# Performance work log

Measured on AMD Instinct MI355X. Metric: run time of the kernel, lower is better.

## Reference

```python
import jax, jax.numpy as jnp
import numpy as np
import math

N = 100000      # nodes
E = 1600000     # edges
D = 128         # in_channels
C = 256         # number of dominant-set cliques
HID = 64        # mlp_hidden
RATIO = 0.8
K = int(math.ceil(RATIO * N))  # 80000 topk nodes per view


def setup_inputs() -> dict:
    key = jax.random.key(0)
    ks = jax.random.split(key, 18)
    s = 0.05
    return {
        "x": jax.random.normal(ks[0], (N, D), jnp.float32),
        "edge_index": jax.random.randint(ks[1], (2, E), 0, N, dtype=jnp.int32),
        "batch": jnp.zeros((N,), jnp.int32),
        "cluster_id": jax.random.randint(ks[2], (N,), 0, C, dtype=jnp.int32),
        # MLP scorer: Linear(D,HID) -> ReLU -> Linear(HID,1)
        "mlp_w1": jax.random.normal(ks[3], (D, HID), jnp.float32) * s,
        "mlp_b1": jnp.zeros((HID,), jnp.float32),
        "mlp_w2": jax.random.normal(ks[4], (HID, 1), jnp.float32) * s,
        "mlp_b2": jnp.zeros((1,), jnp.float32),
        # GATConv(D, 1, heads=1)
        "gat_w": jax.random.normal(ks[5], (D, 1), jnp.float32) * s,
        "gat_a_src": jax.random.normal(ks[6], (1,), jnp.float32) * s,
        "gat_a_dst": jax.random.normal(ks[7], (1,), jnp.float32) * s,
        "gat_b": jnp.zeros((1,), jnp.float32),
        # InterChannelGCN attention Linear(2D,1) split into fine/coarse halves
        "att_w_fine": jax.random.normal(ks[8], (D,), jnp.float32) * s,
        "att_w_coarse": jax.random.normal(ks[9], (D,), jnp.float32) * s,
        "att_b": jnp.zeros((1,), jnp.float32),
        # InterChannelGCN transform Linear(D,D)
        "trans_w": jax.random.normal(ks[10], (D, D), jnp.float32) * s,
        "trans_b": jnp.zeros((D,), jnp.float32),
    }


def _inter_channel_gcn(h_fine, H_coarse, R, wa, wb, ab, tw, tb):
    # attention(Linear(2D,1)) on concat(h_fine_i, H_coarse_j) == h_fine@wa + H_coarse@wb + b
    scores = h_fine @ wa[:, None] + (H_coarse @ wb)[None, :] + ab[0]   # [K, C]
    attn = jax.nn.softmax(scores * R, axis=-1)                          # mask-by-multiply, as original
    out = attn @ H_coarse + h_fine                                      # add_self=True
    return jax.nn.relu(out @ tw + tb)                                   # normalize=False


def reference(x, edge_index, batch, cluster_id,
              mlp_w1, mlp_b1, mlp_w2, mlp_b2,
              gat_w, gat_a_src, gat_a_dst, gat_b,
              att_w_fine, att_w_coarse, att_b, trans_w, trans_b):
    src, dst = edge_index[0], edge_index[1]

    # --- DominantClustering('avg'): cluster means as coarse features ---
    counts = jax.ops.segment_sum(jnp.ones((N,), jnp.float32), cluster_id, num_segments=C)
    Hcoarse = jax.ops.segment_sum(x, cluster_id, num_segments=C) / jnp.maximum(counts, 1.0)[:, None]

    # --- feature view: MLP score + topk ---
    feature_score = (jax.nn.relu(x @ mlp_w1 + mlp_b1) @ mlp_w2 + mlp_b2)[:, 0]   # [N]
    _, feat_idx = jax.lax.top_k(feature_score, K)
    feature_view3 = x[feat_idx]
    R_feat = jax.nn.one_hot(cluster_id[feat_idx], C, dtype=x.dtype)              # relationship matrix
    fuse1 = _inter_channel_gcn(feature_view3, Hcoarse, R_feat,
                               att_w_fine, att_w_coarse, att_b, trans_w, trans_b)

    # --- local view: GATConv(D,1,heads=1) score + topk ---
    h = x @ gat_w                                                                 # [N,1]
    e = jax.nn.leaky_relu(gat_a_src[0] * h[src, 0] + gat_a_dst[0] * h[dst, 0], 0.2)  # [E]
    m = jax.ops.segment_max(e, dst, num_segments=N)
    ex = jnp.exp(e - m[dst])
    den = jax.ops.segment_sum(ex, dst, num_segments=N)
    alpha = ex / jnp.maximum(den[dst], 1e-16)
    localview_score = jax.ops.segment_sum(alpha * h[src, 0], dst, num_segments=N) + gat_b[0]
    _, local_idx = jax.lax.top_k(localview_score, K)
    local_view1 = x[local_idx]
    R_local = jax.nn.one_hot(cluster_id[local_idx], C, dtype=x.dtype)
    fuse2 = _inter_channel_gcn(local_view1, Hcoarse, R_local,
                               att_w_fine, att_w_coarse, att_b, trans_w, trans_b)

    # --- union, edge filtering + remapping (padded fixed shapes) ---
    in_feat = jnp.zeros((N,), bool).at[feat_idx].set(True)
    in_local = jnp.zeros((N,), bool).at[local_idx].set(True)
    union = in_feat | in_local
    mapping = jnp.where(union, jnp.cumsum(union.astype(jnp.int32)) - 1, -1)
    m0, m1 = mapping[src], mapping[dst]
    valid = (m0 >= 0) & (m1 >= 0)
    edge_index_topk = jnp.where(valid[None, :], jnp.stack([m0, m1]), -1)          # [2,E], -1 = dropped

    # --- fused features (faithful to original's fuse1/fuse2 index swap) ---
    A = jnp.zeros((N, D), x.dtype).at[feat_idx].set(fuse2)    # fuse2 indexed by feature topk position
    B = jnp.zeros((N, D), x.dtype).at[local_idx].set(fuse1)   # fuse1 indexed by local topk position
    both = in_feat & in_local
    Fp = jnp.where(both[:, None], (A + B) * 0.5, A + B)
    Fp = jnp.where(union[:, None], Fp, 0.0)                   # [N,D], zero outside union

    new_batch = jnp.where(union, batch, -1)
    return Fp, edge_index_topk, new_batch
```

## Files before the change

### kernel.cpp

```cpp
#include <hip/hip_runtime.h>
#include <hip/hip_bf16.h>
#include <stdint.h>

#define N 100000
#define E_ 1600000
#define D 128
#define C_ 256
#define HID 64
#define KSEL 80000
#define NB 4096
#define CHUNK 1024
#define NCHUNK ((N + CHUNK - 1) / CHUNK)
#define CSEG 32
#define NBK 782
#define BCAP 2560
#define RMAX 2048
#define NSC64 ((N + 63) / 64)
#define EB ((E_ + 255) / 256)
#define ZB ((N * 32 + 255) / 256)

typedef __attribute__((ext_vector_type(8))) short bf16x8;
typedef __attribute__((ext_vector_type(4))) float f32x4;

__device__ __forceinline__ unsigned enc_f(float f) {
  unsigned b = __float_as_uint(f);
  return (b & 0x80000000u) ? ~b : (b | 0x80000000u);
}
__device__ __forceinline__ float dec_f(unsigned u) {
  unsigned b = (u & 0x80000000u) ? (u ^ 0x80000000u) : ~u;
  return __uint_as_float(b);
}

__device__ __forceinline__ unsigned short f2bf(float f) {
  unsigned u = __float_as_uint(f);
  unsigned r = u + 0x7FFFu + ((u >> 16) & 1u);
  return (unsigned short)(r >> 16);
}

__global__ __launch_bounds__(256) void k_hist_cluster(const int* __restrict__ cid, int* __restrict__ ccount) {
  int n = blockIdx.x * 256 + threadIdx.x;
  if (n < N) atomicAdd(&ccount[cid[n]], 1);
}

__global__ __launch_bounds__(1024) void k_scan_small(const int* __restrict__ in0, int* __restrict__ out0, int n) {
  __shared__ int sums[1024];
  const int* in = in0 + (size_t)blockIdx.x * n;
  int* out = out0 + (size_t)blockIdx.x * n;
  int t = threadIdx.x;
  int per = (n + 1023) / 1024;
  int base = t * per;
  int loc = 0;
  for (int k = 0; k < per; ++k) { int i = base + k; if (i < n) loc += in[i]; }
  sums[t] = loc; __syncthreads();
  for (int off = 1; off < 1024; off <<= 1) {
    int v = (t >= off) ? sums[t - off] : 0;
    __syncthreads();
    sums[t] += v;
    __syncthreads();
  }
  int run = (t == 0) ? 0 : sums[t - 1];
  for (int k = 0; k < per; ++k) { int i = base + k; if (i < n) { out[i] = run; run += in[i]; } }
}

__global__ __launch_bounds__(256) void k_scatter_cluster(const int* __restrict__ cid, const int* __restrict__ cstart,
                                                         int* __restrict__ ccur, int* __restrict__ cslot) {
  int n = blockIdx.x * 256 + threadIdx.x;
  if (n < N) {
    int c = cid[n];
    int p = cstart[c] + atomicAdd(&ccur[c], 1);
    cslot[p] = n;
  }
}

__global__ __launch_bounds__(128) void k_cluster_partial(const float* __restrict__ x, const int* __restrict__ cstart,
                                                         const int* __restrict__ ccount, const int* __restrict__ cslot,
                                                         float* __restrict__ Hc) {
  int c = blockIdx.x >> 5;
  int s = blockIdx.x & (CSEG - 1);
  int d = threadIdx.x;
  int st = cstart[c], cnt = ccount[c];
  int seg = (cnt + CSEG - 1) / CSEG;
  int lo = s * seg;
  int hi = min(cnt, lo + seg);
  if (lo >= hi) return;
  float acc = 0.f;
  int k = lo;
  for (; k + 2 <= hi; k += 2) {
    int n0 = cslot[st + k], n1 = cslot[st + k + 1];
    float v0 = x[(size_t)n0 * D + d];
    float v1 = x[(size_t)n1 * D + d];
    acc += v0 + v1;
  }
  if (k < hi) acc += x[(size_t)cslot[st + k] * D + d];
  atomicAdd(&Hc[(size_t)c * D + d], acc);
}

__global__ __launch_bounds__(128) void k_mean_gdot(const int* __restrict__ ccount, const float* __restrict__ wb,
                                                   float* __restrict__ Hc, float* __restrict__ gdot) {
  __shared__ float red[128];
  int c = blockIdx.x, d = threadIdx.x;
  float hv = Hc[(size_t)c * D + d] / (float)max(ccount[c], 1);
  Hc[(size_t)c * D + d] = hv;
  red[d] = hv * wb[d];
  __syncthreads();
  if (d < 64) {
    float v = red[d] + red[d + 64];
    for (int off = 32; off; off >>= 1) v += __shfl_down(v, off);
    if (d == 0) gdot[c] = v;
  }
}

__global__ __launch_bounds__(128) void k_S_SW_HW(const float* __restrict__ Hc, const float* __restrict__ tw,
                                                 float* __restrict__ SW, float* __restrict__ HW,
                                                 unsigned short* __restrict__ twT) {
  __shared__ float Sl[128];
  int b = blockIdx.x, t = threadIdx.x;
  if (b == 0) {
    float s = 0.f;
    for (int c = 0; c < C_; ++c) s += Hc[(size_t)c * D + t];
    Sl[t] = s;
    __syncthreads();
    float acc = 0.f;
    for (int d = 0; d < D; ++d) acc = fmaf(Sl[d], tw[(size_t)d * D + t], acc);
    SW[t] = acc;
  } else if (b <= C_) {
    const float* src = Hc + (size_t)(b - 1) * D;
    float acc = 0.f;
    for (int d = 0; d < D; ++d) acc = fmaf(src[d], tw[(size_t)d * D + t], acc);
    HW[(size_t)(b - 1) * D + t] = acc;
  } else {
    int k = b - C_ - 1;
    twT[(size_t)t * D + k] = f2bf(tw[(size_t)k * D + t]);
  }
}

__global__ __launch_bounds__(256, 4) void k_score64(const float* __restrict__ x, const float* __restrict__ w1,
                                                    const float* __restrict__ b1, const float* __restrict__ w2,
                                                    const float* __restrict__ b2, const float* __restrict__ gw,
                                                    const float* __restrict__ wa, float* __restrict__ scoreF,
                                                    float* __restrict__ hg, float* __restrict__ aDot,
                                                    uint2* __restrict__ pmmF) {
  __shared__ float xld[64 * D];
  int tid = threadIdx.x;
  int base = blockIdx.x * 64;
#pragma unroll
  for (int k = 0; k < 8; ++k) {
    int i = k * 256 + tid;
    int r = i >> 5, cc = i & 31;
    int n = base + r;
    float4 v = make_float4(0.f, 0.f, 0.f, 0.f);
    if (n < N) v = ((const float4*)(x + (size_t)n * D))[cc];
    ((float4*)xld)[r * 32 + (cc ^ (r & 7))] = v;
  }
  __syncthreads();

  int rg = tid >> 4;
  int cg = tid & 15;
  int r0 = rg * 4;
  int c4 = cg * 4;
  float acc[4][4] = {};
  float4 wc0 = *(const float4*)(w1 + (size_t)0 * HID + c4);
  float4 wc1 = *(const float4*)(w1 + (size_t)1 * HID + c4);
  float4 wc2 = *(const float4*)(w1 + (size_t)2 * HID + c4);
  float4 wc3 = *(const float4*)(w1 + (size_t)3 * HID + c4);
  for (int d4 = 0; d4 < D; d4 += 4) {
    float4 wn0, wn1, wn2, wn3;
    if (d4 + 4 < D) {
      wn0 = *(const float4*)(w1 + (size_t)(d4 + 4) * HID + c4);
      wn1 = *(const float4*)(w1 + (size_t)(d4 + 5) * HID + c4);
      wn2 = *(const float4*)(w1 + (size_t)(d4 + 6) * HID + c4);
      wn3 = *(const float4*)(w1 + (size_t)(d4 + 7) * HID + c4);
    } else {
      wn0 = wn1 = wn2 = wn3 = make_float4(0.f, 0.f, 0.f, 0.f);
    }
    int j = d4 >> 2;
#pragma unroll
    for (int rr = 0; rr < 4; ++rr) {
      int row = r0 + rr;
      float4 xv = ((const float4*)xld)[row * 32 + (j ^ (row & 7))];
      acc[rr][0] = fmaf(xv.x, wc0.x, acc[rr][0]);
      acc[rr][1] = fmaf(xv.x, wc0.y, acc[rr][1]);
      acc[rr][2] = fmaf(xv.x, wc0.z, acc[rr][2]);
      acc[rr][3] = fmaf(xv.x, wc0.w, acc[rr][3]);
      acc[rr][0] = fmaf(xv.y, wc1.x, acc[rr][0]);
      acc[rr][1] = fmaf(xv.y, wc1.y, acc[rr][1]);
      acc[rr][2] = fmaf(xv.y, wc1.z, acc[rr][2]);
      acc[rr][3] = fmaf(xv.y, wc1.w, acc[rr][3]);
      acc[rr][0] = fmaf(xv.z, wc2.x, acc[rr][0]);
      acc[rr][1] = fmaf(xv.z, wc2.y, acc[rr][1]);
      acc[rr][2] = fmaf(xv.z, wc2.z, acc[rr][2]);
      acc[rr][3] = fmaf(xv.z, wc2.w, acc[rr][3]);
      acc[rr][0] = fmaf(xv.w, wc3.x, acc[rr][0]);
      acc[rr][1] = fmaf(xv.w, wc3.y, acc[rr][1]);
      acc[rr][2] = fmaf(xv.w, wc3.z, acc[rr][2]);
      acc[rr][3] = fmaf(xv.w, wc3.w, acc[rr][3]);
    }
    wc0 = wn0; wc1 = wn1; wc2 = wn2; wc3 = wn3;
  }

  float4 b1v = *(const float4*)(b1 + c4);
  float4 w2v = *(const float4*)(w2 + c4);
  float bb = b2[0];
  unsigned vmx = 0u, vmn = 0xFFFFFFFFu;
#pragma unroll
  for (int rr = 0; rr < 4; ++rr) {
    float p = fmaxf(acc[rr][0] + b1v.x, 0.f) * w2v.x
            + fmaxf(acc[rr][1] + b1v.y, 0.f) * w2v.y
            + fmaxf(acc[rr][2] + b1v.z, 0.f) * w2v.z
            + fmaxf(acc[rr][3] + b1v.w, 0.f) * w2v.w;
#pragma unroll
    for (int off = 8; off; off >>= 1) p += __shfl_xor(p, off);
    if (cg == 0) {
      int n = base + r0 + rr;
      if (n < N) {
        float sf = p + bb;
        scoreF[n] = sf;
        unsigned e = enc_f(sf);
        vmx = max(vmx, e);
        vmn = min(vmn, e);
      }
    }
  }
#pragma unroll
  for (int off = 32; off; off >>= 1) {
    vmx = max(vmx, (unsigned)__shfl_xor((int)vmx, off));
    vmn = min(vmn, (unsigned)__shfl_xor((int)vmn, off));
  }

  float4 gwa = *(const float4*)(gw + c4);
  float4 gwb = *(const float4*)(gw + 64 + c4);
  float4 waa = *(const float4*)(wa + c4);
  float4 wab = *(const float4*)(wa + 64 + c4);
#pragma unroll
  for (int rr = 0; rr < 4; ++rr) {
    int row = r0 + rr;
    float4 xa = ((const float4*)xld)[row * 32 + (cg ^ (row & 7))];
    float4 xb = ((const float4*)xld)[row * 32 + ((cg + 16) ^ (row & 7))];
    float hp = xa.x * gwa.x + xa.y * gwa.y + xa.z * gwa.z + xa.w * gwa.w
             + xb.x * gwb.x + xb.y * gwb.y + xb.z * gwb.z + xb.w * gwb.w;
    float ap = xa.x * waa.x + xa.y * waa.y + xa.z * waa.z + xa.w * waa.w
             + xb.x * wab.x + xb.y * wab.y + xb.z * wab.z + xb.w * wab.w;
#pragma unroll
    for (int off = 8; off; off >>= 1) {
      hp += __shfl_xor(hp, off);
      ap += __shfl_xor(ap, off);
    }
    if (cg == 0) {
      int n = base + row;
      if (n < N) { hg[n] = hp; aDot[n] = ap; }
    }
  }

  __syncthreads();
  if ((tid & 63) == 0) {
    ((unsigned*)xld)[(tid >> 6) * 2] = vmx;
    ((unsigned*)xld)[(tid >> 6) * 2 + 1] = vmn;
  }
  __syncthreads();
  if (tid == 0) {
    const unsigned* xu = (const unsigned*)xld;
    unsigned a = max(max(xu[0], xu[2]), max(xu[4], xu[6]));
    unsigned b = min(min(xu[1], xu[3]), min(xu[5], xu[7]));
    pmmF[blockIdx.x] = make_uint2(a, b);
  }
}

__global__ __launch_bounds__(1024) void k_escatter(const int* __restrict__ ei, int* __restrict__ gcnt,
                                                   unsigned* __restrict__ payload) {
  __shared__ int lcnt[NBK];
  __shared__ int lbase[NBK];
  int tid = threadIdx.x;
  for (int i = tid; i < NBK; i += 1024) lcnt[i] = 0;
  int e0 = blockIdx.x * 8192;
  int es[8], ed[8];
#pragma unroll
  for (int k = 0; k < 8; ++k) {
    int e = e0 + k * 1024 + tid;
    bool v = (e < E_);
    es[k] = v ? ei[e] : -1;
    ed[k] = v ? ei[E_ + e] : -1;
  }
  __syncthreads();
#pragma unroll
  for (int k = 0; k < 8; ++k)
    if (ed[k] >= 0) atomicAdd(&lcnt[ed[k] >> 7], 1);
  __syncthreads();
  for (int i = tid; i < NBK; i += 1024) {
    int c = lcnt[i];
    lbase[i] = c ? atomicAdd(&gcnt[i], c) : 0;
    lcnt[i] = 0;
  }
  __syncthreads();
#pragma unroll
  for (int k = 0; k < 8; ++k) {
    if (ed[k] < 0) continue;
    int s = es[k], d = ed[k];
    int b = d >> 7, dl = d & 127;
    int pos = lbase[b] + atomicAdd(&lcnt[b], 1);
    if (pos < BCAP) payload[(size_t)b * BCAP + pos] = (unsigned)s | ((unsigned)dl << 24);
  }
}

__global__ __launch_bounds__(256) void k_esoftmax(const unsigned* __restrict__ payload, const int* __restrict__ gcnt,
                                                  const float* __restrict__ hg, const float* __restrict__ asrc,
                                                  const float* __restrict__ adst, const float* __restrict__ gb,
                                                  float* __restrict__ scoreL, uint2* __restrict__ pmmL) {
  __shared__ float dS[128];
  __shared__ float nS[128];
  __shared__ float hgl[128];
  __shared__ unsigned pw[8];
  int b = blockIdx.x;
  int tid = threadIdx.x;
  if (tid < 128) {
    dS[tid] = 0.f; nS[tid] = 0.f;
    int g = b * 128 + tid;
    hgl[tid] = (g < N) ? hg[g] : 0.f;
  }
  __syncthreads();
  float as = asrc[0], ad = adst[0];
  int cnt = min(gcnt[b], BCAP);
  const unsigned* bp = payload + (size_t)b * BCAP;
  for (int i = tid; i < cnt; i += 256) {
    unsigned r = bp[i];
    int s = (int)(r & 0xFFFFFFu), dl = (int)(r >> 24);
    float h = hg[s];
    float z = as * h + ad * hgl[dl];
    float ev = (z > 0.f) ? z : 0.2f * z;
    float ex = expf(ev);
    atomicAdd(&dS[dl], ex);
    atomicAdd(&nS[dl], ex * h);
  }
  __syncthreads();
  unsigned vmx = 0u, vmn = 0xFFFFFFFFu;
  if (tid < 128) {
    int dst = b * 128 + tid;
    if (dst < N) {
      float sl = nS[tid] / fmaxf(dS[tid], 1e-16f) + gb[0];
      scoreL[dst] = sl;
      unsigned e = enc_f(sl);
      vmx = e; vmn = e;
    }
  }
#pragma unroll
  for (int off = 32; off; off >>= 1) {
    vmx = max(vmx, (unsigned)__shfl_xor((int)vmx, off));
    vmn = min(vmn, (unsigned)__shfl_xor((int)vmn, off));
  }
  if ((tid & 63) == 0) { pw[(tid >> 6) * 2] = vmx; pw[(tid >> 6) * 2 + 1] = vmn; }
  __syncthreads();
  if (tid == 0) {
    unsigned a = max(max(pw[0], pw[2]), max(pw[4], pw[6]));
    unsigned c = min(min(pw[1], pw[3]), min(pw[5], pw[7]));
    pmmL[b] = make_uint2(a, c);
  }
}

__global__ __launch_bounds__(1024) void k_mm_reduce(const uint2* __restrict__ pmmF, const uint2* __restrict__ pmmL,
                                                    unsigned* __restrict__ mm) {
  __shared__ unsigned s[4][16];
  int t = threadIdx.x;
  unsigned mxF = 0u, mnF = 0xFFFFFFFFu, mxL = 0u, mnL = 0xFFFFFFFFu;
  for (int i = t; i < NSC64; i += 1024) {
    uint2 v = pmmF[i];
    mxF = max(mxF, v.x); mnF = min(mnF, v.y);
  }
  for (int i = t; i < NBK; i += 1024) {
    uint2 v = pmmL[i];
    mxL = max(mxL, v.x); mnL = min(mnL, v.y);
  }
#pragma unroll
  for (int off = 32; off; off >>= 1) {
    mxF = max(mxF, (unsigned)__shfl_xor((int)mxF, off));
    mnF = min(mnF, (unsigned)__shfl_xor((int)mnF, off));
    mxL = max(mxL, (unsigned)__shfl_xor((int)mxL, off));
    mnL = min(mnL, (unsigned)__shfl_xor((int)mnL, off));
  }
  int w = t >> 6;
  if ((t & 63) == 0) { s[0][w] = mxF; s[1][w] = mnF; s[2][w] = mxL; s[3][w] = mnL; }
  __syncthreads();
  if (t == 0) {
    unsigned a = 0u, b = 0xFFFFFFFFu, c = 0u, d = 0xFFFFFFFFu;
    for (int i = 0; i < 16; ++i) {
      a = max(a, s[0][i]); b = min(b, s[1][i]);
      c = max(c, s[2][i]); d = min(d, s[3][i]);
    }
    mm[0] = a; mm[2] = b; mm[1] = c; mm[3] = d;
  }
}

__global__ __launch_bounds__(256) void k_bucket_hist2(const float* __restrict__ sc2, const unsigned* __restrict__ mm,
                                                      int* __restrict__ bucket2, int* __restrict__ hist2) {
  int v = blockIdx.y;
  int n = blockIdx.x * 256 + threadIdx.x;
  if (n >= N) return;
  const float* sc = sc2 + (size_t)v * N;
  float smax = dec_f(mm[v]), smin = dec_f(mm[2 + v]);
  float range = smax - smin;
  float scale = (range > 0.f) ? ((float)NB / range) : 0.f;
  float t = (smax - sc[n]) * scale;
  int b = (int)t;
  b = b < 0 ? 0 : (b > NB - 1 ? NB - 1 : b);
  bucket2[(size_t)v * N + n] = b;
  atomicAdd(&hist2[v * NB + b], 1);
}

__global__ __launch_bounds__(256) void k_bucket_scatter2(const int* __restrict__ bucket2, const int* __restrict__ start2,
                                                         int* __restrict__ cur2, int* __restrict__ slot2) {
  int v = blockIdx.y;
  int n = blockIdx.x * 256 + threadIdx.x;
  if (n >= N) return;
  int b = bucket2[(size_t)v * N + n];
  slot2[(size_t)v * N + start2[v * NB + b] + atomicAdd(&cur2[v * NB + b], 1)] = n;
}

__global__ __launch_bounds__(64) void k_bucket_rank3(const float* __restrict__ sc2, const int* __restrict__ start2,
                                                     const int* __restrict__ hist2, const int* __restrict__ slot2,
                                                     int* __restrict__ rank2, int* __restrict__ sorted2) {
  __shared__ unsigned long long keys[RMAX];
  int v = blockIdx.y;
  int b = blockIdx.x;
  int st = start2[v * NB + b], cnt = hist2[v * NB + b];
  if (cnt == 0) return;
  const float* sc = sc2 + (size_t)v * N;
  const int* slot = slot2 + (size_t)v * N;
  int* rank = rank2 + (size_t)v * N;
  int* sorted = sorted2 + (size_t)v * N;
  int tid = threadIdx.x;
  if (cnt <= RMAX) {
    for (int i = tid; i < cnt; i += 64) {
      int m = slot[st + i];
      keys[i] = (((unsigned long long)(~enc_f(sc[m]))) << 32) | (unsigned)m;
    }
    __syncthreads();
    for (int i = tid; i < cnt; i += 64) {
      unsigned long long mykey = keys[i];
      int r = 0;
      for (int j = 0; j < cnt; ++j) r += (keys[j] < mykey) ? 1 : 0;
      int m = (int)(mykey & 0xFFFFFFFFu);
      rank[m] = st + r;
      sorted[st + r] = m;
    }
  } else {
    for (int i = tid; i < cnt; i += 64) {
      int m = slot[st + i];
      unsigned long long mykey = (((unsigned long long)(~enc_f(sc[m]))) << 32) | (unsigned)m;
      int r = 0;
      for (int j = 0; j < cnt; ++j) {
        int mj = slot[st + j];
        unsigned long long k = (((unsigned long long)(~enc_f(sc[mj]))) << 32) | (unsigned)mj;
        r += (k < mykey) ? 1 : 0;
      }
      rank[m] = st + r;
      sorted[st + r] = m;
    }
  }
}

__global__ __launch_bounds__(1024) void k_union_chunksum(const int* __restrict__ rankF, const int* __restrict__ rankL,
                                                         int* __restrict__ csum) {
  __shared__ int red[1024];
  int t = threadIdx.x; int i = blockIdx.x * 1024 + t;
  int u = (i < N) ? (((rankF[i] < KSEL) || (rankL[i] < KSEL)) ? 1 : 0) : 0;
  red[t] = u; __syncthreads();
  for (int off = 512; off; off >>= 1) { if (t < off) red[t] += red[t + off]; __syncthreads(); }
  if (t == 0) csum[blockIdx.x] = red[0];
}

__global__ __launch_bounds__(1024) void k_union_map(const int* __restrict__ rankF, const int* __restrict__ rankL,
                                                    const int* __restrict__ cstart, const int* __restrict__ batch,
                                                    int* __restrict__ mapping, float* __restrict__ outBatch) {
  __shared__ int sums[1024];
  int t = threadIdx.x; int i = blockIdx.x * 1024 + t;
  int u = (i < N) ? (((rankF[i] < KSEL) || (rankL[i] < KSEL)) ? 1 : 0) : 0;
  sums[t] = u; __syncthreads();
  for (int off = 1; off < 1024; off <<= 1) {
    int v = (t >= off) ? sums[t - off] : 0;
    __syncthreads();
    sums[t] += v;
    __syncthreads();
  }
  if (i < N) {
    mapping[i] = u ? (cstart[blockIdx.x] + sums[t] - 1) : -1;
    outBatch[i] = u ? (float)batch[i] : -1.0f;
  }
}

__global__ __launch_bounds__(256) void k_edge_zero(const int* __restrict__ ei, const int* __restrict__ mapping,
                                                   float* __restrict__ outE, float* __restrict__ Fp) {
  int b = blockIdx.x;
  if (b < EB) {
    int e = b * 256 + threadIdx.x;
    if (e >= E_) return;
    int m0 = mapping[ei[e]], m1 = mapping[ei[E_ + e]];
    bool valid = (m0 >= 0) && (m1 >= 0);
    outE[e] = valid ? (float)m0 : -1.f;
    outE[E_ + e] = valid ? (float)m1 : -1.f;
  } else {
    int i = (b - EB) * 256 + threadIdx.x;
    int n = i >> 5;
    if (n < N && mapping[n] < 0) ((float4*)Fp)[i] = make_float4(0.f, 0.f, 0.f, 0.f);
  }
}

__global__ __launch_bounds__(256, 4) void k_fuse64(const float* __restrict__ x, const unsigned short* __restrict__ twT,
                                                   const float* __restrict__ tb, const float* __restrict__ SW,
                                                   const float* __restrict__ HW, const float* __restrict__ gdot,
                                                   const float* __restrict__ aDot, const int* __restrict__ cid,
                                                   const int* __restrict__ srcL, const int* __restrict__ tgtL,
                                                   const float* __restrict__ attb, const int* __restrict__ rankF,
                                                   float* __restrict__ Fp, int accum) {
  __shared__ __align__(16) unsigned xw[64 * 64];
  __shared__ float pq[64 * 2];
  __shared__ int mt[64 * 2];
  __shared__ int ft[64];
  int tid = threadIdx.x;
  int base = blockIdx.x * 64;
  if (tid < 64) {
    int ws = srcL[base + tid];
    int cc = cid[ws];
    int tg = tgtL[base + tid];
    mt[tid * 2] = cc;
    mt[tid * 2 + 1] = tg;
    ft[tid] = (rankF[tg] < KSEL) ? 1 : 0;
    float s = aDot[ws] + gdot[cc] + attb[0];
    float mx = fmaxf(s, 0.f);
    float esm = expf(s - mx), eom = expf(-mx);
    float dn = esm + 255.f * eom;
    pq[tid * 2] = esm / dn;
    pq[tid * 2 + 1] = eom / dn;
  }
#pragma unroll
  for (int k = 0; k < 8; ++k) {
    int i = k * 256 + tid;
    int r = i >> 5, c4 = i & 31;
    int ws = srcL[base + r];
    float4 v = ((const float4*)(x + (size_t)ws * D))[c4];
    uint2 pk;
    pk.x = (unsigned)f2bf(v.x) | ((unsigned)f2bf(v.y) << 16);
    pk.y = (unsigned)f2bf(v.z) | ((unsigned)f2bf(v.w) << 16);
    int u2 = r * 32 + (c4 ^ ((r & 7) << 1));
    ((uint2*)xw)[u2] = pk;
  }
  __syncthreads();

  int w = tid >> 6;
  int l = tid & 63;
  int nl = l & 15;
  int khalf = l >> 4;
  int row = w * 16 + nl;

  f32x4 acc[8] = {};
  const char* xbase = (const char*)xw + row * 256;
  unsigned rsw = (unsigned)((row & 7) << 4);
  bf16x8 bfr[4];
#pragma unroll
  for (int ks = 0; ks < 4; ++ks)
    bfr[ks] = *(const bf16x8*)(xbase + (((unsigned)(ks * 64 + khalf * 16)) ^ rsw));
#pragma unroll
  for (int ks = 0; ks < 4; ++ks) {
#pragma unroll
    for (int ot = 0; ot < 8; ++ot) {
      bf16x8 afrag = *(const bf16x8*)(twT + (size_t)(ot * 16 + nl) * D + ks * 32 + khalf * 8);
      acc[ot] = __builtin_amdgcn_mfma_f32_16x16x32_bf16(afrag, bfr[ks], acc[ot], 0, 0, 0);
    }
  }

  float p = pq[row * 2], q = pq[row * 2 + 1];
  int cc = mt[row * 2];
  int tgt = mt[row * 2 + 1];
  int doAcc = accum && ft[row];
#pragma unroll
  for (int ot = 0; ot < 8; ++ot) {
    int ch = ot * 16 + khalf * 4;
    float4 tbv = *(const float4*)(tb + ch);
    float4 swv = *(const float4*)(SW + ch);
    float4 hw = *(const float4*)(HW + (size_t)cc * D + ch);
    float4 o;
    o.x = fmaxf(acc[ot][0] + tbv.x + q * swv.x + (p - q) * hw.x, 0.f);
    o.y = fmaxf(acc[ot][1] + tbv.y + q * swv.y + (p - q) * hw.y, 0.f);
    o.z = fmaxf(acc[ot][2] + tbv.z + q * swv.z + (p - q) * hw.z, 0.f);
    o.w = fmaxf(acc[ot][3] + tbv.w + q * swv.w + (p - q) * hw.w, 0.f);
    float4* dst = (float4*)(Fp + (size_t)tgt * D + ch);
    if (doAcc) {
      float4 old = *dst;
      o.x = (o.x + old.x) * 0.5f;
      o.y = (o.y + old.y) * 0.5f;
      o.z = (o.z + old.z) * 0.5f;
      o.w = (o.w + old.w) * 0.5f;
    }
    *dst = o;
  }
}

extern "C" void kernel_launch(void* const* d_in, const int* in_sizes, int n_in,
                              void* d_out, int out_size, void* d_ws, size_t ws_size,
                              hipStream_t stream) {
  const float* x   = (const float*)d_in[0];
  const int* ei    = (const int*)d_in[1];
  const int* batch = (const int*)d_in[2];
  const int* cid   = (const int*)d_in[3];
  const float* w1  = (const float*)d_in[4];
  const float* b1  = (const float*)d_in[5];
  const float* w2  = (const float*)d_in[6];
  const float* b2  = (const float*)d_in[7];
  const float* gw  = (const float*)d_in[8];
  const float* gas = (const float*)d_in[9];
  const float* gad = (const float*)d_in[10];
  const float* gb  = (const float*)d_in[11];
  const float* wa  = (const float*)d_in[12];
  const float* wb  = (const float*)d_in[13];
  const float* ab  = (const float*)d_in[14];
  const float* tw  = (const float*)d_in[15];
  const float* tb  = (const float*)d_in[16];
  (void)in_sizes; (void)n_in; (void)ws_size; (void)out_size;

  char* p = (char*)d_ws;
  auto alloc = [&](size_t bytes) -> char* {
    char* r = p;
    p += (bytes + 255) & ~(size_t)255;
    return r;
  };
  int* ccount    = (int*)alloc(C_ * 4);
  int* ccur      = (int*)alloc(C_ * 4);
  unsigned* mm   = (unsigned*)alloc(16);
  int* hist2     = (int*)alloc(2 * NB * 4);
  int* cur2      = (int*)alloc(2 * NB * 4);
  float* Hc      = (float*)alloc((size_t)C_ * D * 4);
  int* gcnt      = (int*)alloc(NBK * 4);
  size_t zeroBytes = (size_t)(p - (char*)d_ws);
  int* cstart   = (int*)alloc(C_ * 4);
  int* cslot    = (int*)alloc((size_t)N * 4);
  float* gdot   = (float*)alloc(C_ * 4);
  float* SW     = (float*)alloc(D * 4);
  float* HW     = (float*)alloc((size_t)C_ * D * 4);
  unsigned short* twT = (unsigned short*)alloc((size_t)D * D * 2);
  float* score2 = (float*)alloc((size_t)2 * N * 4);
  float* hg     = (float*)alloc((size_t)N * 4);
  float* aDot   = (float*)alloc((size_t)N * 4);
  unsigned* payload = (unsigned*)alloc((size_t)NBK * BCAP * 4);
  uint2* pmmF   = (uint2*)alloc((size_t)NSC64 * 8);
  uint2* pmmL   = (uint2*)alloc((size_t)NBK * 8);
  int* bucket2  = (int*)alloc((size_t)2 * N * 4);
  int* start2   = (int*)alloc(2 * NB * 4);
  int* slot2    = (int*)alloc((size_t)2 * N * 4);
  int* sorted2  = (int*)alloc((size_t)2 * N * 4);
  int* rank2    = (int*)alloc((size_t)2 * N * 4);
  int* csums    = (int*)alloc(NCHUNK * 4);
  int* cstarts  = (int*)alloc(NCHUNK * 4);
  int* mapping  = (int*)alloc((size_t)N * 4);

  float* scoreF = score2;
  float* scoreL = score2 + N;
  int* sortedF  = sorted2;
  int* sortedL  = sorted2 + N;
  int* rankF    = rank2;
  int* rankL    = rank2 + N;

  float* outF = (float*)d_out;
  float* outE = outF + (size_t)N * D;
  float* outB = outE + (size_t)2 * E_;

  hipMemsetAsync(d_ws, 0, zeroBytes, stream);

  k_hist_cluster<<<(N + 255) / 256, 256, 0, stream>>>(cid, ccount);
  k_scan_small<<<1, 1024, 0, stream>>>(ccount, cstart, C_);
  k_scatter_cluster<<<(N + 255) / 256, 256, 0, stream>>>(cid, cstart, ccur, cslot);
  k_cluster_partial<<<C_ * CSEG, 128, 0, stream>>>(x, cstart, ccount, cslot, Hc);
  k_mean_gdot<<<C_, 128, 0, stream>>>(ccount, wb, Hc, gdot);
  k_S_SW_HW<<<C_ + 1 + D, 128, 0, stream>>>(Hc, tw, SW, HW, twT);

  k_score64<<<NSC64, 256, 0, stream>>>(x, w1, b1, w2, b2, gw, wa, scoreF, hg, aDot, pmmF);
  k_escatter<<<(E_ + 8191) / 8192, 1024, 0, stream>>>(ei, gcnt, payload);
  k_esoftmax<<<NBK, 256, 0, stream>>>(payload, gcnt, hg, gas, gad, gb, scoreL, pmmL);
  k_mm_reduce<<<1, 1024, 0, stream>>>(pmmF, pmmL, mm);

  dim3 g2((N + 255) / 256, 2);
  k_bucket_hist2<<<g2, 256, 0, stream>>>(score2, mm, bucket2, hist2);
  k_scan_small<<<2, 1024, 0, stream>>>(hist2, start2, NB);
  k_bucket_scatter2<<<g2, 256, 0, stream>>>(bucket2, start2, cur2, slot2);
  dim3 gr(NB, 2);
  k_bucket_rank3<<<gr, 64, 0, stream>>>(score2, start2, hist2, slot2, rank2, sorted2);

  k_union_chunksum<<<NCHUNK, 1024, 0, stream>>>(rankF, rankL, csums);
  k_scan_small<<<1, 1024, 0, stream>>>(csums, cstarts, NCHUNK);
  k_union_map<<<NCHUNK, 1024, 0, stream>>>(rankF, rankL, cstarts, batch, mapping, outB);
  k_edge_zero<<<EB + ZB, 256, 0, stream>>>(ei, mapping, outE, outF);

  k_fuse64<<<KSEL / 64, 256, 0, stream>>>(x, twT, tb, SW, HW, gdot, aDot, cid, sortedL, sortedF, ab, rankF, outF, 0);
  k_fuse64<<<KSEL / 64, 256, 0, stream>>>(x, twT, tb, SW, HW, gdot, aDot, cid, sortedF, sortedL, ab, rankF, outF, 1);
}
```

Measured before the change: 520.7 us.

## Fuse two fuse passes into one union-indexed kernel computing both views per node

Builds a compacted list of union nodes during the mapping step. A single kernel then walks that list and, for each target node, computes both the fine and coarse-view transforms and averages them in registers. This replaces two launches, one of which read back the first pass's output for averaging. In exchange, every union node runs both MFMA passes, including nodes that belong to only one view, and shared memory use doubles.

```diff
diff --git a/kernel.cpp b/kernel.cpp
--- a/kernel.cpp
+++ b/kernel.cpp
@@ -468,7 +468,8 @@
 
 __global__ __launch_bounds__(1024) void k_union_map(const int* __restrict__ rankF, const int* __restrict__ rankL,
                                                     const int* __restrict__ cstart, const int* __restrict__ batch,
-                                                    int* __restrict__ mapping, float* __restrict__ outBatch) {
+                                                    int* __restrict__ mapping, float* __restrict__ outBatch,
+                                                    int* __restrict__ ulist) {
   __shared__ int sums[1024];
   int t = threadIdx.x; int i = blockIdx.x * 1024 + t;
   int u = (i < N) ? (((rankF[i] < KSEL) || (rankL[i] < KSEL)) ? 1 : 0) : 0;
@@ -480,7 +481,9 @@
     __syncthreads();
   }
   if (i < N) {
-    mapping[i] = u ? (cstart[blockIdx.x] + sums[t] - 1) : -1;
+    int m_ = u ? (cstart[blockIdx.x] + sums[t] - 1) : -1;
+    mapping[i] = m_;
+    if (u) ulist[m_] = i;
     outBatch[i] = u ? (float)batch[i] : -1.0f;
   }
 }
@@ -502,44 +505,74 @@
   }
 }
 
-__global__ __launch_bounds__(256, 4) void k_fuse64(const float* __restrict__ x, const unsigned short* __restrict__ twT,
-                                                   const float* __restrict__ tb, const float* __restrict__ SW,
-                                                   const float* __restrict__ HW, const float* __restrict__ gdot,
-                                                   const float* __restrict__ aDot, const int* __restrict__ cid,
-                                                   const int* __restrict__ srcL, const int* __restrict__ tgtL,
-                                                   const float* __restrict__ attb, const int* __restrict__ rankF,
-                                                   float* __restrict__ Fp, int accum) {
-  __shared__ __align__(16) unsigned xw[64 * 64];
-  __shared__ float pq[64 * 2];
-  __shared__ int mt[64 * 2];
-  __shared__ int ft[64];
+__global__ __launch_bounds__(256) void k_fuseU(const float* __restrict__ x, const unsigned short* __restrict__ twT,
+                                               const float* __restrict__ tb, const float* __restrict__ SW,
+                                               const float* __restrict__ HW, const float* __restrict__ gdot,
+                                               const float* __restrict__ aDot, const int* __restrict__ cid,
+                                               const int* __restrict__ sortedF, const int* __restrict__ sortedL,
+                                               const int* __restrict__ rankF, const int* __restrict__ rankL,
+                                               const int* __restrict__ ulist, const int* __restrict__ cstarts,
+                                               const int* __restrict__ csums, const float* __restrict__ attb,
+                                               float* __restrict__ Fp) {
+  __shared__ __align__(16) unsigned xwA[64 * 64];
+  __shared__ __align__(16) unsigned xwB[64 * 64];
+  __shared__ float pqA[64 * 2], pqB[64 * 2];
+  __shared__ int mtA[64], mtB[64];
+  __shared__ int tgl[64];
+  __shared__ int fl[64];
+  __shared__ int srcAB[64 * 2];
   int tid = threadIdx.x;
   int base = blockIdx.x * 64;
+  int UC = cstarts[NCHUNK - 1] + csums[NCHUNK - 1];
+  if (base >= UC) return;
   if (tid < 64) {
-    int ws = srcL[base + tid];
-    int cc = cid[ws];
-    int tg = tgtL[base + tid];
-    mt[tid * 2] = cc;
-    mt[tid * 2 + 1] = tg;
-    ft[tid] = (rankF[tg] < KSEL) ? 1 : 0;
-    float s = aDot[ws] + gdot[cc] + attb[0];
-    float mx = fmaxf(s, 0.f);
-    float esm = expf(s - mx), eom = expf(-mx);
-    float dn = esm + 255.f * eom;
-    pq[tid * 2] = esm / dn;
-    pq[tid * 2 + 1] = eom / dn;
-  }
+    int pos = base + tid;
+    int t = (pos < UC) ? ulist[pos] : -1;
+    int ra = (t >= 0) ? rankF[t] : KSEL;
+    int rb = (t >= 0) ? rankL[t] : KSEL;
+    int vA = (ra < KSEL) ? 1 : 0;
+    int vB = (rb < KSEL) ? 1 : 0;
+    int sA = vA ? sortedL[ra] : 0;
+    int sB = vB ? sortedF[rb] : 0;
+    srcAB[tid * 2] = sA;
+    srcAB[tid * 2 + 1] = sB;
+    tgl[tid] = t;
+    fl[tid] = vA | (vB << 1);
+    int cA = cid[sA], cB = cid[sB];
+    mtA[tid] = cA;
+    mtB[tid] = cB;
+    float ab0 = attb[0];
+    float sAv = aDot[sA] + gdot[cA] + ab0;
+    float mxA = fmaxf(sAv, 0.f);
+    float eA = expf(sAv - mxA), oA = expf(-mxA);
+    float dA = eA + 255.f * oA;
+    pqA[tid * 2] = eA / dA;
+    pqA[tid * 2 + 1] = oA / dA;
+    float sBv = aDot[sB] + gdot[cB] + ab0;
+    float mxB = fmaxf(sBv, 0.f);
+    float eB = expf(sBv - mxB), oB = expf(-mxB);
+    float dB = eB + 255.f * oB;
+    pqB[tid * 2] = eB / dB;
+    pqB[tid * 2 + 1] = oB / dB;
+  }
+  __syncthreads();
 #pragma unroll
   for (int k = 0; k < 8; ++k) {
     int i = k * 256 + tid;
     int r = i >> 5, c4 = i & 31;
-    int ws = srcL[base + r];
-    float4 v = ((const float4*)(x + (size_t)ws * D))[c4];
+    int u2 = r * 32 + (c4 ^ ((r & 7) << 1));
+    int wsA = srcAB[r * 2];
+    float4 v = ((const float4*)(x + (size_t)wsA * D))[c4];
     uint2 pk;
     pk.x = (unsigned)f2bf(v.x) | ((unsigned)f2bf(v.y) << 16);
     pk.y = (unsigned)f2bf(v.z) | ((unsigned)f2bf(v.w) << 16);
-    int u2 = r * 32 + (c4 ^ ((r & 7) << 1));
-    ((uint2*)xw)[u2] = pk;
+    ((uint2*)xwA)[u2] = pk;
+    int wsB = srcAB[r * 2 + 1];
+    float4 u = ((const float4*)(x + (size_t)wsB * D))[c4];
+    uint2 pk2;
+    pk2.x = (unsigned)f2bf(u.x) | ((unsigned)f2bf(u.y) << 16);
+    pk2.y = (unsigned)f2bf(u.z) | ((unsigned)f2bf(u.w) << 16);
+    ((uint2*)xwB)[u2] = pk2;
   }
   __syncthreads();
 
@@ -549,46 +582,60 @@
   int khalf = l >> 4;
   int row = w * 16 + nl;
 
-  f32x4 acc[8] = {};
-  const char* xbase = (const char*)xw + row * 256;
+  f32x4 accA[8] = {};
+  f32x4 accB[8] = {};
+  const char* xbA = (const char*)xwA + row * 256;
+  const char* xbB = (const char*)xwB + row * 256;
   unsigned rsw = (unsigned)((row & 7) << 4);
-  bf16x8 bfr[4];
-#pragma unroll
-  for (int ks = 0; ks < 4; ++ks)
-    bfr[ks] = *(const bf16x8*)(xbase + (((unsigned)(ks * 64 + khalf * 16)) ^ rsw));
+  bf16x8 bfrA[4], bfrB[4];
+#pragma unroll
+  for (int ks = 0; ks < 4; ++ks) {
+    unsigned off = ((unsigned)(ks * 64 + khalf * 16)) ^ rsw;
+    bfrA[ks] = *(const bf16x8*)(xbA + off);
+    bfrB[ks] = *(const bf16x8*)(xbB + off);
+  }
 #pragma unroll
   for (int ks = 0; ks < 4; ++ks) {
 #pragma unroll
     for (int ot = 0; ot < 8; ++ot) {
       bf16x8 afrag = *(const bf16x8*)(twT + (size_t)(ot * 16 + nl) * D + ks * 32 + khalf * 8);
-      acc[ot] = __builtin_amdgcn_mfma_f32_16x16x32_bf16(afrag, bfr[ks], acc[ot], 0, 0, 0);
-    }
-  }
-
-  float p = pq[row * 2], q = pq[row * 2 + 1];
-  int cc = mt[row * 2];
-  int tgt = mt[row * 2 + 1];
-  int doAcc = accum && ft[row];
+      accA[ot] = __builtin_amdgcn_mfma_f32_16x16x32_bf16(afrag, bfrA[ks], accA[ot], 0, 0, 0);
+      accB[ot] = __builtin_amdgcn_mfma_f32_16x16x32_bf16(afrag, bfrB[ks], accB[ot], 0, 0, 0);
+    }
+  }
+
+  int t = tgl[row];
+  int f = fl[row];
+  float pA = pqA[row * 2], qA = pqA[row * 2 + 1];
+  float pB = pqB[row * 2], qB = pqB[row * 2 + 1];
+  int cA = mtA[row], cB = mtB[row];
 #pragma unroll
   for (int ot = 0; ot < 8; ++ot) {
     int ch = ot * 16 + khalf * 4;
     float4 tbv = *(const float4*)(tb + ch);
     float4 swv = *(const float4*)(SW + ch);
-    float4 hw = *(const float4*)(HW + (size_t)cc * D + ch);
-    float4 o;
-    o.x = fmaxf(acc[ot][0] + tbv.x + q * swv.x + (p - q) * hw.x, 0.f);
-    o.y = fmaxf(acc[ot][1] + tbv.y + q * swv.y + (p - q) * hw.y, 0.f);
-    o.z = fmaxf(acc[ot][2] + tbv.z + q * swv.z + (p - q) * hw.z, 0.f);
-    o.w = fmaxf(acc[ot][3] + tbv.w + q * swv.w + (p - q) * hw.w, 0.f);
-    float4* dst = (float4*)(Fp + (size_t)tgt * D + ch);
-    if (doAcc) {
-      float4 old = *dst;
-      o.x = (o.x + old.x) * 0.5f;
-      o.y = (o.y + old.y) * 0.5f;
-      o.z = (o.z + old.z) * 0.5f;
-      o.w = (o.w + old.w) * 0.5f;
-    }
-    *dst = o;
+    float4 hwA = *(const float4*)(HW + (size_t)cA * D + ch);
+    float4 hwB = *(const float4*)(HW + (size_t)cB * D + ch);
+    float4 oA, oB, o;
+    oA.x = fmaxf(accA[ot][0] + tbv.x + qA * swv.x + (pA - qA) * hwA.x, 0.f);
+    oA.y = fmaxf(accA[ot][1] + tbv.y + qA * swv.y + (pA - qA) * hwA.y, 0.f);
+    oA.z = fmaxf(accA[ot][2] + tbv.z + qA * swv.z + (pA - qA) * hwA.z, 0.f);
+    oA.w = fmaxf(accA[ot][3] + tbv.w + qA * swv.w + (pA - qA) * hwA.w, 0.f);
+    oB.x = fmaxf(accB[ot][0] + tbv.x + qB * swv.x + (pB - qB) * hwB.x, 0.f);
+    oB.y = fmaxf(accB[ot][1] + tbv.y + qB * swv.y + (pB - qB) * hwB.y, 0.f);
+    oB.z = fmaxf(accB[ot][2] + tbv.z + qB * swv.z + (pB - qB) * hwB.z, 0.f);
+    oB.w = fmaxf(accB[ot][3] + tbv.w + qB * swv.w + (pB - qB) * hwB.w, 0.f);
+    if (f == 3) {
+      o.x = (oA.x + oB.x) * 0.5f;
+      o.y = (oA.y + oB.y) * 0.5f;
+      o.z = (oA.z + oB.z) * 0.5f;
+      o.w = (oA.w + oB.w) * 0.5f;
+    } else if (f & 1) {
+      o = oA;
+    } else {
+      o = oB;
+    }
+    if (t >= 0) *(float4*)(Fp + (size_t)t * D + ch) = o;
   }
 }
 
@@ -648,6 +695,7 @@
   int* csums    = (int*)alloc(NCHUNK * 4);
   int* cstarts  = (int*)alloc(NCHUNK * 4);
   int* mapping  = (int*)alloc((size_t)N * 4);
+  int* ulist    = (int*)alloc((size_t)N * 4);
 
   float* scoreF = score2;
   float* scoreL = score2 + N;
@@ -683,9 +731,10 @@
 
   k_union_chunksum<<<NCHUNK, 1024, 0, stream>>>(rankF, rankL, csums);
   k_scan_small<<<1, 1024, 0, stream>>>(csums, cstarts, NCHUNK);
-  k_union_map<<<NCHUNK, 1024, 0, stream>>>(rankF, rankL, cstarts, batch, mapping, outB);
+  k_union_map<<<NCHUNK, 1024, 0, stream>>>(rankF, rankL, cstarts, batch, mapping, outB, ulist);
   k_edge_zero<<<EB + ZB, 256, 0, stream>>>(ei, mapping, outE, outF);
 
-  k_fuse64<<<KSEL / 64, 256, 0, stream>>>(x, twT, tb, SW, HW, gdot, aDot, cid, sortedL, sortedF, ab, rankF, outF, 0);
-  k_fuse64<<<KSEL / 64, 256, 0, stream>>>(x, twT, tb, SW, HW, gdot, aDot, cid, sortedF, sortedL, ab, rankF, outF, 1);
-}
+  k_fuseU<<<NSC64, 256, 0, stream>>>(x, twT, tb, SW, HW, gdot, aDot, cid,
+                                     sortedF, sortedL, rankF, rankL, ulist,
+                                     cstarts, csums, ab, outF);
+}
```

Result: faster. 495.2 us (-4.9%).
